# Kernel optimization log

Measured on AMD Instinct MI355X. Metric: run time of the kernel, lower is better.

The kernel has to match this reference:

```python
import jax, jax.numpy as jnp
import numpy as np

N_NODES = 30000
N_EDGES = 480000
IN_FEAT = 256
OUT_FEAT = 256
N_RELS = 8
N_HEADS = 4
HEAD_DIM = OUT_FEAT // N_HEADS
LEAKY_SLOPE = 0.2


def setup_inputs() -> dict:
    key = jax.random.key(0)
    ks = jax.random.split(key, 8)
    inputs = jax.random.normal(ks[0], (N_NODES, IN_FEAT), dtype=jnp.float32)
    conv_weights = jax.random.normal(ks[1], (N_RELS, N_HEADS, IN_FEAT, HEAD_DIM), dtype=jnp.float32) * (1.0 / np.sqrt(IN_FEAT))
    attn_l = jax.random.normal(ks[2], (N_RELS, N_HEADS, HEAD_DIM), dtype=jnp.float32) * 0.1
    attn_r = jax.random.normal(ks[3], (N_RELS, N_HEADS, HEAD_DIM), dtype=jnp.float32) * 0.1
    h_bias = jax.random.normal(ks[4], (OUT_FEAT,), dtype=jnp.float32) * 0.02
    edge_src = jax.random.randint(ks[5], (N_EDGES,), 0, N_NODES, dtype=jnp.int32)
    edge_dst = jax.random.randint(ks[6], (N_EDGES,), 0, N_NODES, dtype=jnp.int32)
    edge_type = jax.random.randint(ks[7], (N_EDGES,), 0, N_RELS, dtype=jnp.int32)
    return {"inputs": inputs, "conv_weights": conv_weights, "attn_l": attn_l,
            "attn_r": attn_r, "h_bias": h_bias, "edge_src": edge_src,
            "edge_dst": edge_dst, "edge_type": edge_type}


def reference(inputs, conv_weights, attn_l, attn_r, h_bias, edge_src, edge_dst, edge_type):
    # Per-relation dense transform of all node features: [R, N, H, D]
    feat_all = jnp.einsum('ni,rhid->rnhd', inputs, conv_weights)
    # Gather transformed source/destination features per edge: [E, H, D]
    feat_src_e = feat_all[edge_type, edge_src]
    feat_dst_e = feat_all[edge_type, edge_dst]
    # Per-edge attention logits (relation-specific attn vectors): [E, H]
    el = jnp.sum(feat_src_e * attn_l[edge_type], axis=-1)
    er = jnp.sum(feat_dst_e * attn_r[edge_type], axis=-1)
    e = jax.nn.leaky_relu(el + er, negative_slope=LEAKY_SLOPE)
    # Segment softmax over incoming edges of each destination node
    m = jax.ops.segment_max(e, edge_dst, num_segments=N_NODES)  # [N, H]
    ex = jnp.exp(e - m[edge_dst])
    denom = jax.ops.segment_sum(ex, edge_dst, num_segments=N_NODES)  # [N, H]
    alpha = ex / denom[edge_dst]  # [E, H]
    # Attention-weighted aggregation of transformed source features
    h = jax.ops.segment_sum(alpha[..., None] * feat_src_e, edge_dst, num_segments=N_NODES)  # [N, H, D]
    h = h.reshape(N_NODES, OUT_FEAT) + h_bias
    # activation=None, self_loop=False, dropout=0.0 (eval) -> identity
    return h
```

## Files before the change

### kernel.cpp

```cpp
#include <hip/hip_runtime.h>
#include <hip/hip_bf16.h>

#define N_NODES 30000
#define NPAD    30080
#define N_EDGES 480000
#define N_RELS  8
#define NB_SCAN 118

typedef short bf16x8 __attribute__((ext_vector_type(8)));
typedef float f32x4  __attribute__((ext_vector_type(4)));

__device__ __forceinline__ unsigned short f2bf(float f) {
    unsigned u = __float_as_uint(f);
    u += 0x7fffu + ((u >> 16) & 1u);
    return (unsigned short)(u >> 16);
}
__device__ __forceinline__ float bf2f(unsigned short h) {
    return __uint_as_float(((unsigned)h) << 16);
}
__device__ __forceinline__ ushort2 pk2bf(float a, float b) {
    __hip_bfloat162 t = __float22bfloat162_rn(float2{a, b});
    union { __hip_bfloat162 h; ushort2 u; } cv; cv.h = t; return cv.u;
}

__device__ __forceinline__ void load_lds16(const void* g, void* l) {
    __builtin_amdgcn_global_load_lds(
        (const __attribute__((address_space(1))) unsigned int*)g,
        (__attribute__((address_space(3))) unsigned int*)l,
        16, 0, 0);
}

__global__ void prep_kernel(const float* __restrict__ x, unsigned short* __restrict__ xbf,
                            const float* __restrict__ cw, unsigned short* __restrict__ wt,
                            const int* __restrict__ edst, int* __restrict__ counts) {
    int b = blockIdx.x;
    if (b < 3760) {
        int t = b * 256 + threadIdx.x;
        int base = t * 8;
        int n = base >> 8;
        unsigned short h[8];
        if (n < N_NODES) {
            float4 a = *(const float4*)(x + base);
            float4 c = *(const float4*)(x + base + 4);
            h[0]=f2bf(a.x); h[1]=f2bf(a.y); h[2]=f2bf(a.z); h[3]=f2bf(a.w);
            h[4]=f2bf(c.x); h[5]=f2bf(c.y); h[6]=f2bf(c.z); h[7]=f2bf(c.w);
        } else {
            #pragma unroll
            for (int i = 0; i < 8; ++i) h[i] = 0;
        }
        uint4 o;
        o.x = (unsigned)h[0] | ((unsigned)h[1] << 16);
        o.y = (unsigned)h[2] | ((unsigned)h[3] << 16);
        o.z = (unsigned)h[4] | ((unsigned)h[5] << 16);
        o.w = (unsigned)h[6] | ((unsigned)h[7] << 16);
        *(uint4*)(xbf + base) = o;
    } else if (b < 5808) {
        int o = (b - 3760) * 256 + threadIdx.x;
        int i = o & 255;
        int c = (o >> 8) & 255;
        int r = o >> 16;
        float v = cw[(((size_t)r * 4 + (c >> 6)) * 256 + i) * 64 + (c & 63)];
        wt[o] = f2bf(v);
    } else {
        int e = (b - 5808) * 256 + threadIdx.x;
        if (e < N_EDGES) atomicAdd(&counts[edst[e]], 1);
    }
}

__global__ void scan1_kernel(const int* __restrict__ counts, int* __restrict__ locexcl,
                             int* __restrict__ bsum) {
    __shared__ int sm[256];
    int tid = threadIdx.x;
    int idx = blockIdx.x * 256 + tid;
    int v = (idx < N_NODES) ? counts[idx] : 0;
    sm[tid] = v;
    __syncthreads();
    for (int o = 1; o < 256; o <<= 1) {
        int t = (tid >= o) ? sm[tid - o] : 0;
        __syncthreads();
        sm[tid] += t;
        __syncthreads();
    }
    int incl = sm[tid];
    if (idx < N_NODES) locexcl[idx] = incl - v;
    if (tid == 255) bsum[blockIdx.x] = incl;
}

__global__ void scan2_kernel(const int* __restrict__ bsum, int* __restrict__ bpre) {
    __shared__ int sm[128];
    int tid = threadIdx.x;
    int v = (tid < NB_SCAN) ? bsum[tid] : 0;
    sm[tid] = v;
    __syncthreads();
    for (int o = 1; o < 128; o <<= 1) {
        int t = (tid >= o) ? sm[tid - o] : 0;
        __syncthreads();
        sm[tid] += t;
        __syncthreads();
    }
    if (tid < NB_SCAN) bpre[tid] = sm[tid] - v;
}

__global__ void scan3_kernel(const int* __restrict__ locexcl, const int* __restrict__ bpre,
                             int* __restrict__ offsets, int* __restrict__ cursor) {
    int idx = blockIdx.x * 256 + threadIdx.x;
    if (idx < N_NODES) {
        int o = bpre[blockIdx.x] + locexcl[idx];
        offsets[idx] = o;
        cursor[idx]  = o;
    }
    if (idx == 0) offsets[N_NODES] = N_EDGES;
}

__global__ __launch_bounds__(256) void gemm_kernel(
    const unsigned short* __restrict__ xbf,
    const unsigned short* __restrict__ wt,
    const float* __restrict__ attn_l,
    const float* __restrict__ attn_r,
    unsigned short* __restrict__ feat,
    float* __restrict__ projl,
    float* __restrict__ projr)
{
    __shared__ __align__(16) unsigned char smem[32768];

    const int tid  = threadIdx.x;
    const int lane = tid & 63;
    const int w    = tid >> 6;
    const int wm   = w >> 1;
    const int wn   = w & 1;
    const int quad = lane >> 4;
    const int l15  = lane & 15;

    const int bid  = blockIdx.x;
    const int work = (bid & 7) * 470 + (bid >> 3);
    const int mt   = work >> 4;
    const int r    = (work >> 1) & 7;
    const int nt   = work & 1;
    const int mbase = mt * 128;
    const int nbase = nt * 128;

    const unsigned short* Asrc = xbf + (size_t)mbase * 256;
    const unsigned short* Bsrc = wt + ((size_t)r * 256 + nbase) * 256;

    f32x4 acc[4][4] = {};

    const int srow = w * 16 + (lane >> 2);
    const int c0   = lane & 3;

    for (int k0 = 0; k0 < 256; k0 += 32) {
        #pragma unroll
        for (int n = 0; n < 2; ++n) {
            int row = n * 64 + srow;
            int c   = c0 ^ ((row >> 1) & 3);
            load_lds16(Asrc + (size_t)row * 256 + k0 + c * 8, smem + (n * 256 + w * 64) * 16);
        }
        #pragma unroll
        for (int n = 0; n < 2; ++n) {
            int row = n * 64 + srow;
            int c   = c0 ^ ((row >> 1) & 3);
            load_lds16(Bsrc + (size_t)row * 256 + k0 + c * 8, smem + 8192 + (n * 256 + w * 64) * 16);
        }
        __syncthreads();

        bf16x8 xf[4], wf[4];
        #pragma unroll
        for (int j = 0; j < 4; ++j) {
            int row = wm * 64 + j * 16 + l15;
            int cc  = quad ^ ((row >> 1) & 3);
            xf[j] = *(const bf16x8*)(smem + row * 64 + cc * 16);
        }
        #pragma unroll
        for (int i = 0; i < 4; ++i) {
            int row = wn * 64 + i * 16 + l15;
            int cc  = quad ^ ((row >> 1) & 3);
            wf[i] = *(const bf16x8*)(smem + 8192 + row * 64 + cc * 16);
        }

        #pragma unroll
        for (int i = 0; i < 4; ++i)
            #pragma unroll
            for (int j = 0; j < 4; ++j)
                acc[i][j] = __builtin_amdgcn_mfma_f32_16x16x32_bf16(wf[i], xf[j], acc[i][j], 0, 0, 0);
        __syncthreads();
    }

    #pragma unroll
    for (int j = 0; j < 4; ++j) {
        int node = mbase + wm * 64 + j * 16 + l15;
        size_t rowb = ((size_t)r * NPAD + node) * 256 + nbase + wn * 64;
        #pragma unroll
        for (int i = 0; i < 4; ++i) {
            ushort2 lo = pk2bf(acc[i][j][0], acc[i][j][1]);
            ushort2 hi = pk2bf(acc[i][j][2], acc[i][j][3]);
            ushort4 v;
            v.x = lo.x; v.y = lo.y; v.z = hi.x; v.w = hi.y;
            *(ushort4*)(feat + rowb + i * 16 + quad * 4) = v;
        }
    }

    const int head = nt * 2 + wn;
    float alv[4][4], arv[4][4];
    #pragma unroll
    for (int i = 0; i < 4; ++i)
        #pragma unroll
        for (int e = 0; e < 4; ++e) {
            int c = i * 16 + quad * 4 + e;
            alv[i][e] = attn_l[((size_t)r * 4 + head) * 64 + c];
            arv[i][e] = attn_r[((size_t)r * 4 + head) * 64 + c];
        }
    float* bufL = (float*)smem + w * 1024;
    float* bufR = (float*)(smem + 16384) + w * 1024;
    #pragma unroll
    for (int j = 0; j < 4; ++j) {
        float s1 = 0.f, s2 = 0.f;
        #pragma unroll
        for (int i = 0; i < 4; ++i)
            #pragma unroll
            for (int e = 0; e < 4; ++e) {
                s1 += acc[i][j][e] * alv[i][e];
                s2 += acc[i][j][e] * arv[i][e];
            }
        int node = j * 16 + l15;
        bufL[node * 5 + quad] = s1;
        bufR[node * 5 + quad] = s2;
    }
    float sL = 0.f, sR = 0.f;
    #pragma unroll
    for (int q = 0; q < 4; ++q) {
        sL += bufL[lane * 5 + q];
        sR += bufR[lane * 5 + q];
    }
    int g = mbase + wm * 64 + lane;
    projl[((size_t)r * NPAD + g) * 4 + head] = sL;
    projr[((size_t)r * NPAD + g) * 4 + head] = sR;
}

__global__ void logits_scatter_kernel(
    const int* __restrict__ esrc, const int* __restrict__ edst, const int* __restrict__ etyp,
    const float* __restrict__ projl, const float* __restrict__ projr,
    int* __restrict__ cursor, int* __restrict__ srcoff, float* __restrict__ exw)
{
    int e = blockIdx.x * 256 + threadIdx.x;
    if (e >= N_EDGES) return;
    int s = esrc[e], d = edst[e], t = etyp[e];
    float4 pl = ((const float4*)projl)[(size_t)t * NPAD + s];
    float4 pr = ((const float4*)projr)[(size_t)t * NPAD + d];
    float4 o;
    float v;
    v = pl.x + pr.x; v = v > 0.f ? v : 0.2f * v; o.x = __expf(v);
    v = pl.y + pr.y; v = v > 0.f ? v : 0.2f * v; o.y = __expf(v);
    v = pl.z + pr.z; v = v > 0.f ? v : 0.2f * v; o.z = __expf(v);
    v = pl.w + pr.w; v = v > 0.f ? v : 0.2f * v; o.w = __expf(v);
    int p = atomicAdd(&cursor[d], 1);
    srcoff[p] = t * NPAD + s;
    ((float4*)exw)[p] = o;
}

__global__ __launch_bounds__(256) void aggregate_kernel(
    const int* __restrict__ offsets, const int* __restrict__ srcoff,
    const float* __restrict__ exw, const unsigned short* __restrict__ feat,
    const float* __restrict__ bias, float* __restrict__ out)
{
    __shared__ float sm[2][64][5];
    int wid  = threadIdx.x >> 6;
    int slot = wid >> 1;
    int half = wid & 1;
    int v = blockIdx.x * 2 + slot;
    int lane = threadIdx.x & 63;
    int head = lane >> 4;
    int s0 = offsets[v], s1 = offsets[v + 1];
    int mid = s0 + ((s1 - s0 + 1) >> 1);
    int lo = half ? mid : s0;
    int hi = half ? s1  : mid;
    float a0 = 0.f, a1 = 0.f, a2 = 0.f, a3 = 0.f, den = 0.f;
    int i = lo;
    for (; i + 8 <= hi; i += 8) {
        int o[8]; float ee[8]; ushort4 ff[8];
        #pragma unroll
        for (int u = 0; u < 8; ++u) { o[u] = srcoff[i + u]; ee[u] = exw[(size_t)(i + u) * 4 + head]; }
        #pragma unroll
        for (int u = 0; u < 8; ++u) ff[u] = *(const ushort4*)(feat + (size_t)o[u] * 256 + lane * 4);
        #pragma unroll
        for (int u = 0; u < 8; ++u) {
            den += ee[u];
            a0 += ee[u] * bf2f(ff[u].x);
            a1 += ee[u] * bf2f(ff[u].y);
            a2 += ee[u] * bf2f(ff[u].z);
            a3 += ee[u] * bf2f(ff[u].w);
        }
    }
    for (; i + 4 <= hi; i += 4) {
        int o[4]; float ee[4]; ushort4 ff[4];
        #pragma unroll
        for (int u = 0; u < 4; ++u) { o[u] = srcoff[i + u]; ee[u] = exw[(size_t)(i + u) * 4 + head]; }
        #pragma unroll
        for (int u = 0; u < 4; ++u) ff[u] = *(const ushort4*)(feat + (size_t)o[u] * 256 + lane * 4);
        #pragma unroll
        for (int u = 0; u < 4; ++u) {
            den += ee[u];
            a0 += ee[u] * bf2f(ff[u].x);
            a1 += ee[u] * bf2f(ff[u].y);
            a2 += ee[u] * bf2f(ff[u].z);
            a3 += ee[u] * bf2f(ff[u].w);
        }
    }
    for (; i + 2 <= hi; i += 2) {
        int o[2]; float ee[2]; ushort4 ff[2];
        #pragma unroll
        for (int u = 0; u < 2; ++u) { o[u] = srcoff[i + u]; ee[u] = exw[(size_t)(i + u) * 4 + head]; }
        #pragma unroll
        for (int u = 0; u < 2; ++u) ff[u] = *(const ushort4*)(feat + (size_t)o[u] * 256 + lane * 4);
        #pragma unroll
        for (int u = 0; u < 2; ++u) {
            den += ee[u];
            a0 += ee[u] * bf2f(ff[u].x);
            a1 += ee[u] * bf2f(ff[u].y);
            a2 += ee[u] * bf2f(ff[u].z);
            a3 += ee[u] * bf2f(ff[u].w);
        }
    }
    if (i < hi) {
        int o0 = srcoff[i];
        float e0 = exw[(size_t)i * 4 + head];
        ushort4 f0 = *(const ushort4*)(feat + (size_t)o0 * 256 + lane * 4);
        den += e0;
        a0 += e0 * bf2f(f0.x);
        a1 += e0 * bf2f(f0.y);
        a2 += e0 * bf2f(f0.z);
        a3 += e0 * bf2f(f0.w);
    }
    if (half) {
        sm[slot][lane][0] = a0; sm[slot][lane][1] = a1;
        sm[slot][lane][2] = a2; sm[slot][lane][3] = a3;
        sm[slot][lane][4] = den;
    }
    __syncthreads();
    if (!half) {
        a0 += sm[slot][lane][0]; a1 += sm[slot][lane][1];
        a2 += sm[slot][lane][2]; a3 += sm[slot][lane][3];
        den += sm[slot][lane][4];
        float inv = den > 0.f ? 1.f / den : 0.f;
        float4 o;
        o.x = a0 * inv + bias[lane * 4 + 0];
        o.y = a1 * inv + bias[lane * 4 + 1];
        o.z = a2 * inv + bias[lane * 4 + 2];
        o.w = a3 * inv + bias[lane * 4 + 3];
        ((float4*)out)[(size_t)v * 64 + lane] = o;
    }
}

extern "C" void kernel_launch(void* const* d_in, const int* in_sizes, int n_in,
                              void* d_out, int out_size, void* d_ws, size_t ws_size,
                              hipStream_t stream) {
    const float* x    = (const float*)d_in[0];
    const float* cw   = (const float*)d_in[1];
    const float* al   = (const float*)d_in[2];
    const float* ar   = (const float*)d_in[3];
    const float* bias = (const float*)d_in[4];
    const int* esrc   = (const int*)d_in[5];
    const int* edst   = (const int*)d_in[6];
    const int* etyp   = (const int*)d_in[7];
    float* out        = (float*)d_out;

    char* ws = (char*)d_ws;
    size_t off = 0;
    auto alloc = [&](size_t bytes) { size_t o = off; off += (bytes + 255) & ~(size_t)255; return o; };

    unsigned short* xbf  = (unsigned short*)(ws + alloc((size_t)NPAD * 256 * 2));
    unsigned short* wt   = (unsigned short*)(ws + alloc((size_t)N_RELS * 256 * 256 * 2));
    unsigned short* feat = (unsigned short*)(ws + alloc((size_t)N_RELS * NPAD * 256 * 2));
    float* projl = (float*)(ws + alloc((size_t)N_RELS * NPAD * 4 * 4));
    float* projr = (float*)(ws + alloc((size_t)N_RELS * NPAD * 4 * 4));
    float* exw   = (float*)(ws + alloc((size_t)N_EDGES * 4 * 4));
    int* srcoff  = (int*)(ws + alloc((size_t)N_EDGES * 4));
    int* counts  = (int*)(ws + alloc((size_t)N_NODES * 4));
    int* offsets = (int*)(ws + alloc((size_t)(N_NODES + 1) * 4));
    int* cursor  = (int*)(ws + alloc((size_t)N_NODES * 4));
    int* locexcl = (int*)(ws + alloc((size_t)N_NODES * 4));
    int* bsum    = (int*)(ws + alloc((size_t)NB_SCAN * 4));
    int* bpre    = (int*)(ws + alloc((size_t)NB_SCAN * 4));

    hipMemsetAsync(counts, 0, (size_t)N_NODES * 4, stream);

    prep_kernel<<<7683, 256, 0, stream>>>(x, xbf, cw, wt, edst, counts);
    scan1_kernel<<<NB_SCAN, 256, 0, stream>>>(counts, locexcl, bsum);
    scan2_kernel<<<1, 128, 0, stream>>>(bsum, bpre);
    scan3_kernel<<<NB_SCAN, 256, 0, stream>>>(locexcl, bpre, offsets, cursor);
    gemm_kernel<<<3760, 256, 0, stream>>>(xbf, wt, al, ar, feat, projl, projr);
    logits_scatter_kernel<<<1875, 256, 0, stream>>>(esrc, edst, etyp, projl, projr,
                                                    cursor, srcoff, exw);
    aggregate_kernel<<<15000, 256, 0, stream>>>(offsets, srcoff, exw, feat, bias, out);
}
```

Before: 258.0 us.

## Restructure GEMM into 256x256 tiles with triple-buffered LDS pipeline

Rewrites the per-relation bf16 GEMM so each 512-thread block computes a 256-node by 256-column tile (all heads of one relation) instead of 128x128. Loads go through a three-stage LDS ring buffer with explicit vmcnt waits and raw barriers, and MFMA sections run at raised wave priority, so global loads overlap compute. NPAD grows to a multiple of 256, which means more padding rows in prep and the workspace. The larger tiles reuse each loaded X and W tile more, at the cost of 96KB LDS and more registers per block, which may limit occupancy.

```diff
diff --git a/kernel.cpp b/kernel.cpp
--- a/kernel.cpp
+++ b/kernel.cpp
@@ -2,7 +2,7 @@
 #include <hip/hip_bf16.h>
 
 #define N_NODES 30000
-#define NPAD    30080
+#define NPAD    30208
 #define N_EDGES 480000
 #define N_RELS  8
 #define NB_SCAN 118
@@ -34,7 +34,7 @@
                             const float* __restrict__ cw, unsigned short* __restrict__ wt,
                             const int* __restrict__ edst, int* __restrict__ counts) {
     int b = blockIdx.x;
-    if (b < 3760) {
+    if (b < 3776) {
         int t = b * 256 + threadIdx.x;
         int base = t * 8;
         int n = base >> 8;
@@ -54,15 +54,15 @@
         o.z = (unsigned)h[4] | ((unsigned)h[5] << 16);
         o.w = (unsigned)h[6] | ((unsigned)h[7] << 16);
         *(uint4*)(xbf + base) = o;
-    } else if (b < 5808) {
-        int o = (b - 3760) * 256 + threadIdx.x;
+    } else if (b < 5824) {
+        int o = (b - 3776) * 256 + threadIdx.x;
         int i = o & 255;
         int c = (o >> 8) & 255;
         int r = o >> 16;
         float v = cw[(((size_t)r * 4 + (c >> 6)) * 256 + i) * 64 + (c & 63)];
         wt[o] = f2bf(v);
     } else {
-        int e = (b - 5808) * 256 + threadIdx.x;
+        int e = (b - 5824) * 256 + threadIdx.x;
         if (e < N_EDGES) atomicAdd(&counts[edst[e]], 1);
     }
 }
@@ -112,7 +112,7 @@
     if (idx == 0) offsets[N_NODES] = N_EDGES;
 }
 
-__global__ __launch_bounds__(256) void gemm_kernel(
+__global__ __launch_bounds__(512, 2) void gemm_kernel(
     const unsigned short* __restrict__ xbf,
     const unsigned short* __restrict__ wt,
     const float* __restrict__ attn_l,
@@ -121,73 +121,106 @@
     float* __restrict__ projl,
     float* __restrict__ projr)
 {
-    __shared__ __align__(16) unsigned char smem[32768];
+    __shared__ __align__(16) unsigned char smem[98304];
 
     const int tid  = threadIdx.x;
     const int lane = tid & 63;
     const int w    = tid >> 6;
-    const int wm   = w >> 1;
-    const int wn   = w & 1;
+    const int wm   = w >> 2;
+    const int wn   = w & 3;
     const int quad = lane >> 4;
     const int l15  = lane & 15;
 
     const int bid  = blockIdx.x;
-    const int work = (bid & 7) * 470 + (bid >> 3);
-    const int mt   = work >> 4;
-    const int r    = (work >> 1) & 7;
-    const int nt   = work & 1;
-    const int mbase = mt * 128;
-    const int nbase = nt * 128;
-
-    const unsigned short* Asrc = xbf + (size_t)mbase * 256;
-    const unsigned short* Bsrc = wt + ((size_t)r * 256 + nbase) * 256;
-
-    f32x4 acc[4][4] = {};
-
-    const int srow = w * 16 + (lane >> 2);
-    const int c0   = lane & 3;
-
-    for (int k0 = 0; k0 < 256; k0 += 32) {
-        #pragma unroll
-        for (int n = 0; n < 2; ++n) {
-            int row = n * 64 + srow;
-            int c   = c0 ^ ((row >> 1) & 3);
-            load_lds16(Asrc + (size_t)row * 256 + k0 + c * 8, smem + (n * 256 + w * 64) * 16);
-        }
-        #pragma unroll
-        for (int n = 0; n < 2; ++n) {
-            int row = n * 64 + srow;
-            int c   = c0 ^ ((row >> 1) & 3);
-            load_lds16(Bsrc + (size_t)row * 256 + k0 + c * 8, smem + 8192 + (n * 256 + w * 64) * 16);
-        }
-        __syncthreads();
-
-        bf16x8 xf[4], wf[4];
-        #pragma unroll
-        for (int j = 0; j < 4; ++j) {
-            int row = wm * 64 + j * 16 + l15;
-            int cc  = quad ^ ((row >> 1) & 3);
-            xf[j] = *(const bf16x8*)(smem + row * 64 + cc * 16);
-        }
-        #pragma unroll
-        for (int i = 0; i < 4; ++i) {
-            int row = wn * 64 + i * 16 + l15;
-            int cc  = quad ^ ((row >> 1) & 3);
-            wf[i] = *(const bf16x8*)(smem + 8192 + row * 64 + cc * 16);
-        }
-
-        #pragma unroll
-        for (int i = 0; i < 4; ++i)
+    const int work = (bid & 7) * 118 + (bid >> 3);
+    const int mt   = work >> 3;
+    const int r    = work & 7;
+    const int mbase = mt * 256;
+
+    const unsigned short* Xg = xbf + (size_t)mbase * 256;
+    const unsigned short* Wg = wt + (size_t)r * 65536;
+
+    unsigned char* Xs = smem;
+    unsigned char* Ws = smem + 49152;
+
+    const int srow_in = lane >> 2;
+    const int schk    = lane & 3;
+
+    auto stage_half = [&](const unsigned short* g, int grow0, int k0, unsigned char* lb) {
+        int row = w * 16 + srow_in;
+        int gc  = schk ^ ((row >> 1) & 3);
+        load_lds16(g + (size_t)(grow0 + row) * 256 + k0 + gc * 8, lb + w * 1024);
+    };
+    auto stage_tile = [&](int T) {
+        int k0 = T * 32;
+        int bb = T % 3;
+        unsigned char* xbuf = Xs + bb * 16384;
+        unsigned char* wbuf = Ws + bb * 16384;
+        stage_half(Xg, 0,   k0, xbuf);
+        stage_half(Xg, 128, k0, xbuf + 8192);
+        stage_half(Wg, 0,   k0, wbuf);
+        stage_half(Wg, 128, k0, wbuf + 8192);
+    };
+
+    f32x4 acc[4][8] = {};
+
+    stage_tile(0);
+    stage_tile(1);
+    stage_tile(2);
+
+    #pragma unroll
+    for (int T = 0; T < 8; ++T) {
+        if (T < 6)      asm volatile("s_waitcnt vmcnt(8)" ::: "memory");
+        else if (T == 6) asm volatile("s_waitcnt vmcnt(4)" ::: "memory");
+        else             asm volatile("s_waitcnt vmcnt(0)" ::: "memory");
+        asm volatile("s_barrier" ::: "memory");
+
+        const unsigned char* xb = Xs + (T % 3) * 16384 + wm * 8192;
+        const unsigned char* wb = Ws + (T % 3) * 16384;
+
+        bf16x8 xf[8], wf2[2];
+        #pragma unroll
+        for (int j = 0; j < 8; ++j) {
+            int rr = j * 16 + l15;
+            xf[j] = *(const bf16x8*)(xb + rr * 64 + (quad ^ ((rr >> 1) & 3)) * 16);
+        }
+        #pragma unroll
+        for (int i = 0; i < 2; ++i) {
+            int fr = wn * 64 + i * 16 + l15;
+            int rr = fr & 127;
+            wf2[i] = *(const bf16x8*)(wb + (fr >> 7) * 8192 + rr * 64 + (quad ^ ((rr >> 1) & 3)) * 16);
+        }
+        __builtin_amdgcn_s_setprio(1);
+        #pragma unroll
+        for (int i = 0; i < 2; ++i)
             #pragma unroll
-            for (int j = 0; j < 4; ++j)
-                acc[i][j] = __builtin_amdgcn_mfma_f32_16x16x32_bf16(wf[i], xf[j], acc[i][j], 0, 0, 0);
-        __syncthreads();
+            for (int j = 0; j < 8; ++j)
+                acc[i][j] = __builtin_amdgcn_mfma_f32_16x16x32_bf16(wf2[i], xf[j], acc[i][j], 0, 0, 0);
+        __builtin_amdgcn_s_setprio(0);
+        asm volatile("s_barrier" ::: "memory");
+
+        #pragma unroll
+        for (int i = 0; i < 2; ++i) {
+            int fr = wn * 64 + (2 + i) * 16 + l15;
+            int rr = fr & 127;
+            wf2[i] = *(const bf16x8*)(wb + (fr >> 7) * 8192 + rr * 64 + (quad ^ ((rr >> 1) & 3)) * 16);
+        }
+        __builtin_amdgcn_s_setprio(1);
+        #pragma unroll
+        for (int i = 0; i < 2; ++i)
+            #pragma unroll
+            for (int j = 0; j < 8; ++j)
+                acc[2 + i][j] = __builtin_amdgcn_mfma_f32_16x16x32_bf16(wf2[i], xf[j], acc[2 + i][j], 0, 0, 0);
+        __builtin_amdgcn_s_setprio(0);
+        asm volatile("s_barrier" ::: "memory");
+
+        if (T < 5) stage_tile(T + 3);
     }
 
     #pragma unroll
-    for (int j = 0; j < 4; ++j) {
-        int node = mbase + wm * 64 + j * 16 + l15;
-        size_t rowb = ((size_t)r * NPAD + node) * 256 + nbase + wn * 64;
+    for (int j = 0; j < 8; ++j) {
+        int node = mbase + wm * 128 + j * 16 + l15;
+        size_t rowb = ((size_t)r * NPAD + node) * 256 + wn * 64;
         #pragma unroll
         for (int i = 0; i < 4; ++i) {
             ushort2 lo = pk2bf(acc[i][j][0], acc[i][j][1]);
@@ -198,20 +231,19 @@
         }
     }
 
-    const int head = nt * 2 + wn;
     float alv[4][4], arv[4][4];
     #pragma unroll
     for (int i = 0; i < 4; ++i)
         #pragma unroll
         for (int e = 0; e < 4; ++e) {
             int c = i * 16 + quad * 4 + e;
-            alv[i][e] = attn_l[((size_t)r * 4 + head) * 64 + c];
-            arv[i][e] = attn_r[((size_t)r * 4 + head) * 64 + c];
-        }
-    float* bufL = (float*)smem + w * 1024;
-    float* bufR = (float*)(smem + 16384) + w * 1024;
+            alv[i][e] = attn_l[((size_t)r * 4 + wn) * 64 + c];
+            arv[i][e] = attn_r[((size_t)r * 4 + wn) * 64 + c];
+        }
+    float* bufL = (float*)smem + w * 640;
+    float* bufR = (float*)(smem + 49152) + w * 640;
     #pragma unroll
-    for (int j = 0; j < 4; ++j) {
+    for (int j = 0; j < 8; ++j) {
         float s1 = 0.f, s2 = 0.f;
         #pragma unroll
         for (int i = 0; i < 4; ++i)
@@ -224,15 +256,16 @@
         bufL[node * 5 + quad] = s1;
         bufR[node * 5 + quad] = s2;
     }
-    float sL = 0.f, sR = 0.f;
     #pragma unroll
-    for (int q = 0; q < 4; ++q) {
-        sL += bufL[lane * 5 + q];
-        sR += bufR[lane * 5 + q];
-    }
-    int g = mbase + wm * 64 + lane;
-    projl[((size_t)r * NPAD + g) * 4 + head] = sL;
-    projr[((size_t)r * NPAD + g) * 4 + head] = sR;
+    for (int h = 0; h < 2; ++h) {
+        int node = h * 64 + lane;
+        float sL = 0.f, sR = 0.f;
+        #pragma unroll
+        for (int q = 0; q < 4; ++q) { sL += bufL[node * 5 + q]; sR += bufR[node * 5 + q]; }
+        int g = mbase + wm * 128 + node;
+        projl[((size_t)r * NPAD + g) * 4 + wn] = sL;
+        projr[((size_t)r * NPAD + g) * 4 + wn] = sR;
+    }
 }
 
 __global__ void logits_scatter_kernel(
@@ -382,11 +415,11 @@
 
     hipMemsetAsync(counts, 0, (size_t)N_NODES * 4, stream);
 
-    prep_kernel<<<7683, 256, 0, stream>>>(x, xbf, cw, wt, edst, counts);
+    prep_kernel<<<7699, 256, 0, stream>>>(x, xbf, cw, wt, edst, counts);
     scan1_kernel<<<NB_SCAN, 256, 0, stream>>>(counts, locexcl, bsum);
     scan2_kernel<<<1, 128, 0, stream>>>(bsum, bpre);
     scan3_kernel<<<NB_SCAN, 256, 0, stream>>>(locexcl, bpre, offsets, cursor);
-    gemm_kernel<<<3760, 256, 0, stream>>>(xbf, wt, al, ar, feat, projl, projr);
+    gemm_kernel<<<944, 512, 0, stream>>>(xbf, wt, al, ar, feat, projl, projr);
     logits_scatter_kernel<<<1875, 256, 0, stream>>>(esrc, edst, etyp, projl, projr,
                                                     cursor, srcoff, exw);
     aggregate_kernel<<<15000, 256, 0, stream>>>(offsets, srcoff, exw, feat, bias, out);
```

Measured after the change: 262.4 us. No clear change (+1.7%).

## Fuse edge logit computation into aggregation and shrink GEMM M-tile to 64

Applied to the files above, without the earlier changes.

Drops the per-edge exw buffer. The scatter kernel now stores only a packed relation and source offset. The aggregate kernel recomputes leaky-relu and exp from projl/projr gathers per edge, which removes a 7.7MB write and read in exchange for an extra gather and exp per lane. The GEMM M-tile is halved to 64 rows with smaller LDS and launch_bounds(256,4) for higher occupancy, and NPAD is enlarged to match. Scatter no longer depends on the GEMM output, so it runs before it.

```diff
diff --git a/kernel.cpp b/kernel.cpp
--- a/kernel.cpp
+++ b/kernel.cpp
@@ -2,7 +2,7 @@
 #include <hip/hip_bf16.h>
 
 #define N_NODES 30000
-#define NPAD    30080
+#define NPAD    30208
 #define N_EDGES 480000
 #define N_RELS  8
 #define NB_SCAN 118
@@ -34,7 +34,7 @@
                             const float* __restrict__ cw, unsigned short* __restrict__ wt,
                             const int* __restrict__ edst, int* __restrict__ counts) {
     int b = blockIdx.x;
-    if (b < 3760) {
+    if (b < 3776) {
         int t = b * 256 + threadIdx.x;
         int base = t * 8;
         int n = base >> 8;
@@ -54,15 +54,15 @@
         o.z = (unsigned)h[4] | ((unsigned)h[5] << 16);
         o.w = (unsigned)h[6] | ((unsigned)h[7] << 16);
         *(uint4*)(xbf + base) = o;
-    } else if (b < 5808) {
-        int o = (b - 3760) * 256 + threadIdx.x;
+    } else if (b < 5824) {
+        int o = (b - 3776) * 256 + threadIdx.x;
         int i = o & 255;
         int c = (o >> 8) & 255;
         int r = o >> 16;
         float v = cw[(((size_t)r * 4 + (c >> 6)) * 256 + i) * 64 + (c & 63)];
         wt[o] = f2bf(v);
     } else {
-        int e = (b - 5808) * 256 + threadIdx.x;
+        int e = (b - 5824) * 256 + threadIdx.x;
         if (e < N_EDGES) atomicAdd(&counts[edst[e]], 1);
     }
 }
@@ -112,7 +112,18 @@
     if (idx == 0) offsets[N_NODES] = N_EDGES;
 }
 
-__global__ __launch_bounds__(256) void gemm_kernel(
+__global__ void scatter_kernel(
+    const int* __restrict__ esrc, const int* __restrict__ edst, const int* __restrict__ etyp,
+    int* __restrict__ cursor, int* __restrict__ srcoff)
+{
+    int e = blockIdx.x * 256 + threadIdx.x;
+    if (e >= N_EDGES) return;
+    int s = esrc[e], d = edst[e], t = etyp[e];
+    int p = atomicAdd(&cursor[d], 1);
+    srcoff[p] = (t << 28) | (t * NPAD + s);
+}
+
+__global__ __launch_bounds__(256, 4) void gemm_kernel(
     const unsigned short* __restrict__ xbf,
     const unsigned short* __restrict__ wt,
     const float* __restrict__ attn_l,
@@ -121,7 +132,7 @@
     float* __restrict__ projl,
     float* __restrict__ projr)
 {
-    __shared__ __align__(16) unsigned char smem[32768];
+    __shared__ __align__(16) unsigned char smem[12288];
 
     const int tid  = threadIdx.x;
     const int lane = tid & 63;
@@ -132,61 +143,59 @@
     const int l15  = lane & 15;
 
     const int bid  = blockIdx.x;
-    const int work = (bid & 7) * 470 + (bid >> 3);
+    const int work = (bid & 7) * 944 + (bid >> 3);
     const int mt   = work >> 4;
     const int r    = (work >> 1) & 7;
     const int nt   = work & 1;
-    const int mbase = mt * 128;
+    const int mbase = mt * 64;
     const int nbase = nt * 128;
 
     const unsigned short* Asrc = xbf + (size_t)mbase * 256;
     const unsigned short* Bsrc = wt + ((size_t)r * 256 + nbase) * 256;
 
-    f32x4 acc[4][4] = {};
+    f32x4 acc[4][2] = {};
 
     const int srow = w * 16 + (lane >> 2);
     const int c0   = lane & 3;
 
     for (int k0 = 0; k0 < 256; k0 += 32) {
+        {
+            int c = c0 ^ ((srow >> 1) & 3);
+            load_lds16(Asrc + (size_t)srow * 256 + k0 + c * 8, smem + w * 1024);
+        }
         #pragma unroll
         for (int n = 0; n < 2; ++n) {
             int row = n * 64 + srow;
             int c   = c0 ^ ((row >> 1) & 3);
-            load_lds16(Asrc + (size_t)row * 256 + k0 + c * 8, smem + (n * 256 + w * 64) * 16);
-        }
-        #pragma unroll
-        for (int n = 0; n < 2; ++n) {
-            int row = n * 64 + srow;
-            int c   = c0 ^ ((row >> 1) & 3);
-            load_lds16(Bsrc + (size_t)row * 256 + k0 + c * 8, smem + 8192 + (n * 256 + w * 64) * 16);
-        }
-        __syncthreads();
-
-        bf16x8 xf[4], wf[4];
-        #pragma unroll
-        for (int j = 0; j < 4; ++j) {
-            int row = wm * 64 + j * 16 + l15;
-            int cc  = quad ^ ((row >> 1) & 3);
-            xf[j] = *(const bf16x8*)(smem + row * 64 + cc * 16);
+            load_lds16(Bsrc + (size_t)row * 256 + k0 + c * 8, smem + 4096 + (n * 256 + w * 64) * 16);
+        }
+        __syncthreads();
+
+        bf16x8 xf[2], wf[4];
+        #pragma unroll
+        for (int j = 0; j < 2; ++j) {
+            int rr = wm * 32 + j * 16 + l15;
+            int cc = quad ^ ((rr >> 1) & 3);
+            xf[j] = *(const bf16x8*)(smem + rr * 64 + cc * 16);
         }
         #pragma unroll
         for (int i = 0; i < 4; ++i) {
-            int row = wn * 64 + i * 16 + l15;
-            int cc  = quad ^ ((row >> 1) & 3);
-            wf[i] = *(const bf16x8*)(smem + 8192 + row * 64 + cc * 16);
+            int rr = wn * 64 + i * 16 + l15;
+            int cc = quad ^ ((rr >> 1) & 3);
+            wf[i] = *(const bf16x8*)(smem + 4096 + rr * 64 + cc * 16);
         }
 
         #pragma unroll
         for (int i = 0; i < 4; ++i)
             #pragma unroll
-            for (int j = 0; j < 4; ++j)
+            for (int j = 0; j < 2; ++j)
                 acc[i][j] = __builtin_amdgcn_mfma_f32_16x16x32_bf16(wf[i], xf[j], acc[i][j], 0, 0, 0);
         __syncthreads();
     }
 
     #pragma unroll
-    for (int j = 0; j < 4; ++j) {
-        int node = mbase + wm * 64 + j * 16 + l15;
+    for (int j = 0; j < 2; ++j) {
+        int node = mbase + wm * 32 + j * 16 + l15;
         size_t rowb = ((size_t)r * NPAD + node) * 256 + nbase + wn * 64;
         #pragma unroll
         for (int i = 0; i < 4; ++i) {
@@ -208,10 +217,10 @@
             alv[i][e] = attn_l[((size_t)r * 4 + head) * 64 + c];
             arv[i][e] = attn_r[((size_t)r * 4 + head) * 64 + c];
         }
-    float* bufL = (float*)smem + w * 1024;
-    float* bufR = (float*)(smem + 16384) + w * 1024;
+    float* bufL = (float*)smem + w * 160;
+    float* bufR = (float*)(smem + 4096) + w * 160;
     #pragma unroll
-    for (int j = 0; j < 4; ++j) {
+    for (int j = 0; j < 2; ++j) {
         float s1 = 0.f, s2 = 0.f;
         #pragma unroll
         for (int i = 0; i < 4; ++i)
@@ -224,41 +233,20 @@
         bufL[node * 5 + quad] = s1;
         bufR[node * 5 + quad] = s2;
     }
-    float sL = 0.f, sR = 0.f;
-    #pragma unroll
-    for (int q = 0; q < 4; ++q) {
-        sL += bufL[lane * 5 + q];
-        sR += bufR[lane * 5 + q];
-    }
-    int g = mbase + wm * 64 + lane;
-    projl[((size_t)r * NPAD + g) * 4 + head] = sL;
-    projr[((size_t)r * NPAD + g) * 4 + head] = sR;
-}
-
-__global__ void logits_scatter_kernel(
-    const int* __restrict__ esrc, const int* __restrict__ edst, const int* __restrict__ etyp,
-    const float* __restrict__ projl, const float* __restrict__ projr,
-    int* __restrict__ cursor, int* __restrict__ srcoff, float* __restrict__ exw)
-{
-    int e = blockIdx.x * 256 + threadIdx.x;
-    if (e >= N_EDGES) return;
-    int s = esrc[e], d = edst[e], t = etyp[e];
-    float4 pl = ((const float4*)projl)[(size_t)t * NPAD + s];
-    float4 pr = ((const float4*)projr)[(size_t)t * NPAD + d];
-    float4 o;
-    float v;
-    v = pl.x + pr.x; v = v > 0.f ? v : 0.2f * v; o.x = __expf(v);
-    v = pl.y + pr.y; v = v > 0.f ? v : 0.2f * v; o.y = __expf(v);
-    v = pl.z + pr.z; v = v > 0.f ? v : 0.2f * v; o.z = __expf(v);
-    v = pl.w + pr.w; v = v > 0.f ? v : 0.2f * v; o.w = __expf(v);
-    int p = atomicAdd(&cursor[d], 1);
-    srcoff[p] = t * NPAD + s;
-    ((float4*)exw)[p] = o;
+    if (lane < 32) {
+        float sL = 0.f, sR = 0.f;
+        #pragma unroll
+        for (int q = 0; q < 4; ++q) { sL += bufL[lane * 5 + q]; sR += bufR[lane * 5 + q]; }
+        int g = mbase + wm * 32 + lane;
+        projl[((size_t)r * NPAD + g) * 4 + head] = sL;
+        projr[((size_t)r * NPAD + g) * 4 + head] = sR;
+    }
 }
 
 __global__ __launch_bounds__(256) void aggregate_kernel(
     const int* __restrict__ offsets, const int* __restrict__ srcoff,
-    const float* __restrict__ exw, const unsigned short* __restrict__ feat,
+    const float* __restrict__ projl, const float* __restrict__ projr,
+    const unsigned short* __restrict__ feat,
     const float* __restrict__ bias, float* __restrict__ out)
 {
     __shared__ float sm[2][64][5];
@@ -272,62 +260,69 @@
     int mid = s0 + ((s1 - s0 + 1) >> 1);
     int lo = half ? mid : s0;
     int hi = half ? s1  : mid;
+    const int vb = v * 4 + head;
     float a0 = 0.f, a1 = 0.f, a2 = 0.f, a3 = 0.f, den = 0.f;
     int i = lo;
     for (; i + 8 <= hi; i += 8) {
-        int o[8]; float ee[8]; ushort4 ff[8];
-        #pragma unroll
-        for (int u = 0; u < 8; ++u) { o[u] = srcoff[i + u]; ee[u] = exw[(size_t)(i + u) * 4 + head]; }
-        #pragma unroll
-        for (int u = 0; u < 8; ++u) ff[u] = *(const ushort4*)(feat + (size_t)o[u] * 256 + lane * 4);
+        int so[8]; float pl[8], pr[8]; ushort4 ff[8];
+        #pragma unroll
+        for (int u = 0; u < 8; ++u) so[u] = srcoff[i + u];
         #pragma unroll
         for (int u = 0; u < 8; ++u) {
-            den += ee[u];
-            a0 += ee[u] * bf2f(ff[u].x);
-            a1 += ee[u] * bf2f(ff[u].y);
-            a2 += ee[u] * bf2f(ff[u].z);
-            a3 += ee[u] * bf2f(ff[u].w);
+            int pidx = so[u] & 0x0FFFFFFF;
+            pl[u] = projl[(size_t)pidx * 4 + head];
+            pr[u] = projr[(size_t)(so[u] >> 28) * (NPAD * 4) + vb];
+            ff[u] = *(const ushort4*)(feat + (size_t)pidx * 256 + lane * 4);
+        }
+        #pragma unroll
+        for (int u = 0; u < 8; ++u) {
+            float lv = pl[u] + pr[u];
+            lv = lv > 0.f ? lv : 0.2f * lv;
+            float ee = __expf(lv);
+            den += ee;
+            a0 += ee * bf2f(ff[u].x);
+            a1 += ee * bf2f(ff[u].y);
+            a2 += ee * bf2f(ff[u].z);
+            a3 += ee * bf2f(ff[u].w);
         }
     }
     for (; i + 4 <= hi; i += 4) {
-        int o[4]; float ee[4]; ushort4 ff[4];
-        #pragma unroll
-        for (int u = 0; u < 4; ++u) { o[u] = srcoff[i + u]; ee[u] = exw[(size_t)(i + u) * 4 + head]; }
-        #pragma unroll
-        for (int u = 0; u < 4; ++u) ff[u] = *(const ushort4*)(feat + (size_t)o[u] * 256 + lane * 4);
+        int so[4]; float pl[4], pr[4]; ushort4 ff[4];
+        #pragma unroll
+        for (int u = 0; u < 4; ++u) so[u] = srcoff[i + u];
         #pragma unroll
         for (int u = 0; u < 4; ++u) {
-            den += ee[u];
-            a0 += ee[u] * bf2f(ff[u].x);
-            a1 += ee[u] * bf2f(ff[u].y);
-            a2 += ee[u] * bf2f(ff[u].z);
-            a3 += ee[u] * bf2f(ff[u].w);
-        }
-    }
-    for (; i + 2 <= hi; i += 2) {
-        int o[2]; float ee[2]; ushort4 ff[2];
-        #pragma unroll
-        for (int u = 0; u < 2; ++u) { o[u] = srcoff[i + u]; ee[u] = exw[(size_t)(i + u) * 4 + head]; }
-        #pragma unroll
-        for (int u = 0; u < 2; ++u) ff[u] = *(const ushort4*)(feat + (size_t)o[u] * 256 + lane * 4);
-        #pragma unroll
-        for (int u = 0; u < 2; ++u) {
-            den += ee[u];
-            a0 += ee[u] * bf2f(ff[u].x);
-            a1 += ee[u] * bf2f(ff[u].y);
-            a2 += ee[u] * bf2f(ff[u].z);
-            a3 += ee[u] * bf2f(ff[u].w);
-        }
-    }
-    if (i < hi) {
-        int o0 = srcoff[i];
-        float e0 = exw[(size_t)i * 4 + head];
-        ushort4 f0 = *(const ushort4*)(feat + (size_t)o0 * 256 + lane * 4);
-        den += e0;
-        a0 += e0 * bf2f(f0.x);
-        a1 += e0 * bf2f(f0.y);
-        a2 += e0 * bf2f(f0.z);
-        a3 += e0 * bf2f(f0.w);
+            int pidx = so[u] & 0x0FFFFFFF;
+            pl[u] = projl[(size_t)pidx * 4 + head];
+            pr[u] = projr[(size_t)(so[u] >> 28) * (NPAD * 4) + vb];
+            ff[u] = *(const ushort4*)(feat + (size_t)pidx * 256 + lane * 4);
+        }
+        #pragma unroll
+        for (int u = 0; u < 4; ++u) {
+            float lv = pl[u] + pr[u];
+            lv = lv > 0.f ? lv : 0.2f * lv;
+            float ee = __expf(lv);
+            den += ee;
+            a0 += ee * bf2f(ff[u].x);
+            a1 += ee * bf2f(ff[u].y);
+            a2 += ee * bf2f(ff[u].z);
+            a3 += ee * bf2f(ff[u].w);
+        }
+    }
+    for (; i < hi; ++i) {
+        int so0 = srcoff[i];
+        int pidx = so0 & 0x0FFFFFFF;
+        float pl0 = projl[(size_t)pidx * 4 + head];
+        float pr0 = projr[(size_t)(so0 >> 28) * (NPAD * 4) + vb];
+        ushort4 f0 = *(const ushort4*)(feat + (size_t)pidx * 256 + lane * 4);
+        float lv = pl0 + pr0;
+        lv = lv > 0.f ? lv : 0.2f * lv;
+        float ee = __expf(lv);
+        den += ee;
+        a0 += ee * bf2f(f0.x);
+        a1 += ee * bf2f(f0.y);
+        a2 += ee * bf2f(f0.z);
+        a3 += ee * bf2f(f0.w);
     }
     if (half) {
         sm[slot][lane][0] = a0; sm[slot][lane][1] = a1;
@@ -371,7 +366,6 @@
     unsigned short* feat = (unsigned short*)(ws + alloc((size_t)N_RELS * NPAD * 256 * 2));
     float* projl = (float*)(ws + alloc((size_t)N_RELS * NPAD * 4 * 4));
     float* projr = (float*)(ws + alloc((size_t)N_RELS * NPAD * 4 * 4));
-    float* exw   = (float*)(ws + alloc((size_t)N_EDGES * 4 * 4));
     int* srcoff  = (int*)(ws + alloc((size_t)N_EDGES * 4));
     int* counts  = (int*)(ws + alloc((size_t)N_NODES * 4));
     int* offsets = (int*)(ws + alloc((size_t)(N_NODES + 1) * 4));
@@ -382,12 +376,11 @@
 
     hipMemsetAsync(counts, 0, (size_t)N_NODES * 4, stream);
 
-    prep_kernel<<<7683, 256, 0, stream>>>(x, xbf, cw, wt, edst, counts);
+    prep_kernel<<<7699, 256, 0, stream>>>(x, xbf, cw, wt, edst, counts);
     scan1_kernel<<<NB_SCAN, 256, 0, stream>>>(counts, locexcl, bsum);
     scan2_kernel<<<1, 128, 0, stream>>>(bsum, bpre);
     scan3_kernel<<<NB_SCAN, 256, 0, stream>>>(locexcl, bpre, offsets, cursor);
-    gemm_kernel<<<3760, 256, 0, stream>>>(xbf, wt, al, ar, feat, projl, projr);
-    logits_scatter_kernel<<<1875, 256, 0, stream>>>(esrc, edst, etyp, projl, projr,
-                                                    cursor, srcoff, exw);
-    aggregate_kernel<<<15000, 256, 0, stream>>>(offsets, srcoff, exw, feat, bias, out);
-}
+    scatter_kernel<<<1875, 256, 0, stream>>>(esrc, edst, etyp, cursor, srcoff);
+    gemm_kernel<<<7552, 256, 0, stream>>>(xbf, wt, al, ar, feat, projl, projr);
+    aggregate_kernel<<<15000, 256, 0, stream>>>(offsets, srcoff, projl, projr, feat, bias, out);
+}
```

After: 272.4 us. 5.6% more time.
